# Performance work log

Hardware: AMD Instinct MI355X
Metric: run time of the kernel (lower is better)

Reference implementation:

```python
import jax, jax.numpy as jnp
import numpy as np

B, N, K = 2, 8192, 16
D_IN, D_OUT = 32, 128
EPS = 1e-5


def _bn(x, gamma, beta):
    # x: (B, C, L); BatchNorm1d training-mode stats over (B, L)
    mean = x.mean(axis=(0, 2), keepdims=True)
    var = x.var(axis=(0, 2), keepdims=True)
    return gamma[None, :, None] * (x - mean) * jax.lax.rsqrt(var + EPS) + beta[None, :, None]


def _shared_mlp(x, w, b, gamma, beta, act):
    # SharedMLP: 1x1 Conv1d (channel GEMM) + BN + activation. x: (B, Cin, L)
    y = jnp.einsum('oi,bil->bol', w, x) + b[None, :, None]
    return act(_bn(y, gamma, beta))


def _attentive_pool(x, w, b):
    # x: (B, C, N, K); per-(b,n,k) Linear over C, softmax over K, weighted sum over K
    scores = jnp.einsum('oc,bcnk->bonk', w, x) + b[None, :, None, None]
    scores = jax.nn.softmax(scores, axis=-1)
    return jnp.sum(scores * x, axis=-1)  # (B, C, N)  (torch keeps K=1 dim; squeezed by SharedMLP reshape)


def _knn(coords, k):
    # brute-force squared-L2 KNN excluding self (faiss IndexFlatL2 semantics)
    sq = jnp.sum(coords * coords, axis=-1)  # (B, N)
    d2 = sq[:, :, None] + sq[:, None, :] - 2.0 * jnp.einsum('bid,bjd->bij', coords, coords)
    n = coords.shape[1]
    d2 = jnp.where(jnp.eye(n, dtype=bool)[None], jnp.inf, d2)
    neg, idx = jax.lax.top_k(-d2, k)  # ascending squared distance
    return idx, jnp.maximum(-neg, 0.0)


def _lse(coords, features, idx, dist, w, b, gamma, beta):
    # LocalSpatialEncoding: gather neighbor coords, build 10-ch relative features, MLP, concat
    Bq, Nq, Kq = idx.shape
    neighbor = jax.vmap(lambda c, i: c[i])(coords, idx)  # (B, N, K, 3)
    center = jnp.broadcast_to(coords[:, :, None, :], neighbor.shape)
    rel = center - neighbor
    spatial = jnp.concatenate([center, neighbor, rel, dist[..., None]], axis=-1)  # (B, N, K, 10)
    spatial = spatial.transpose(0, 3, 1, 2).reshape(Bq, 10, Nq * Kq)
    sf = _shared_mlp(spatial, w, b, gamma, beta, jax.nn.relu).reshape(Bq, -1, Nq, Kq)
    feat = jnp.broadcast_to(features[..., None], (Bq, features.shape[1], Nq, Kq))
    return jnp.concatenate([sf, feat], axis=1)


def _forward(coords, features,
             mlp1_w, mlp1_b, mlp1_g, mlp1_bt,
             lse1_w, lse1_b, lse1_g, lse1_bt,
             mlpp1_w, mlpp1_b, mlpp1_g, mlpp1_bt,
             lse2_w, lse2_b, lse2_g, lse2_bt,
             mlp2_w, mlp2_b, mlp2_g, mlp2_bt,
             res_w, res_b, res_g, res_bt,
             pool1_w, pool1_b, pool2_w, pool2_b):
    # faiss output is detached in torch (numpy round-trip) -> stop_gradient
    idx, dist = _knn(jax.lax.stop_gradient(coords), K)
    lrelu02 = lambda v: jnp.where(v >= 0, v, 0.2 * v)   # LeakyReLU(0.2)
    lrelu01 = lambda v: jnp.where(v >= 0, v, 0.01 * v)  # default LeakyReLU
    x = _shared_mlp(features, mlp1_w, mlp1_b, mlp1_g, mlp1_bt, lrelu02)      # (B, 64, N)
    x = _lse(coords, x, idx, dist, lse1_w, lse1_b, lse1_g, lse1_bt)          # (B, 128, N, K)
    x = _attentive_pool(x, pool1_w, pool1_b)                                  # (B, 128, N)
    x = _shared_mlp(x, mlpp1_w, mlpp1_b, mlpp1_g, mlpp1_bt, jax.nn.relu)     # (B, 32, N)
    x = _lse(coords, x, idx, dist, lse2_w, lse2_b, lse2_g, lse2_bt)          # (B, 64, N, K)
    x = _attentive_pool(x, pool2_w, pool2_b)                                  # (B, 64, N)
    x_main = _shared_mlp(x, mlp2_w, mlp2_b, mlp2_g, mlp2_bt, jax.nn.relu)    # (B, 128, N)
    resid = _shared_mlp(features, res_w, res_b, res_g, res_bt, jax.nn.relu)  # (B, 128, N)
    return lrelu01(jnp.concatenate([x_main, resid], axis=1))                 # (B, 256, N)


def setup_inputs() -> dict:
    key = jax.random.key(0)
    ks = iter(jax.random.split(key, 64))

    def lin(ci, co):
        w = jax.random.normal(next(ks), (co, ci), jnp.float32) / np.float32(np.sqrt(ci))
        b = jax.random.normal(next(ks), (co,), jnp.float32) * 0.01
        return w, b

    inp = {}
    inp['coords'] = jax.random.normal(next(ks), (B, N, 3), jnp.float32)
    inp['features'] = jax.random.normal(next(ks), (B, D_IN, N), jnp.float32)
    for name, ci, co in [('mlp1', D_IN, D_OUT // 2), ('lse1', 10, D_OUT // 2),
                         ('mlpp1', D_OUT, D_OUT // 4), ('lse2', 10, D_OUT // 4),
                         ('mlp2', D_OUT // 2, D_OUT), ('res', D_IN, D_OUT)]:
        w, b = lin(ci, co)
        inp[name + '_w'], inp[name + '_b'] = w, b
        inp[name + '_g'] = jnp.ones((co,), jnp.float32)
        inp[name + '_bt'] = jnp.zeros((co,), jnp.float32)
    for name, c in [('pool1', D_OUT), ('pool2', D_OUT // 2)]:
        w, b = lin(c, c)
        inp[name + '_w'], inp[name + '_b'] = w, b
    return inp


def reference(coords, features,
              mlp1_w, mlp1_b, mlp1_g, mlp1_bt,
              lse1_w, lse1_b, lse1_g, lse1_bt,
              mlpp1_w, mlpp1_b, mlpp1_g, mlpp1_bt,
              lse2_w, lse2_b, lse2_g, lse2_bt,
              mlp2_w, mlp2_b, mlp2_g, mlp2_bt,
              res_w, res_b, res_g, res_bt,
              pool1_w, pool1_b, pool2_w, pool2_b):
    return _forward(coords, features,
                    mlp1_w, mlp1_b, mlp1_g, mlp1_bt,
                    lse1_w, lse1_b, lse1_g, lse1_bt,
                    mlpp1_w, mlpp1_b, mlpp1_g, mlpp1_bt,
                    lse2_w, lse2_b, lse2_g, lse2_bt,
                    mlp2_w, mlp2_b, mlp2_g, mlp2_bt,
                    res_w, res_b, res_g, res_bt,
                    pool1_w, pool1_b, pool2_w, pool2_b)
```

## Files before the change

### kernel.cpp

```cpp
#include <hip/hip_runtime.h>

static constexpr int N_ = 8192;
static constexpr int B_ = 2;
static constexpr int K_ = 16;

typedef __attribute__((ext_vector_type(8))) short bf16x8;
typedef __attribute__((ext_vector_type(4))) float f32x4;

__device__ __forceinline__ short f2bf(float f) {
  unsigned int u = __float_as_uint(f);
  unsigned int r = (u + 0x7FFFu + ((u >> 16) & 1u)) >> 16;
  return (short)r;
}
__device__ __forceinline__ float bf2f(short h) {
  return __uint_as_float(((unsigned int)(unsigned short)h) << 16);
}

__global__ __launch_bounds__(512) void knn_kernel(const float* __restrict__ coords,
                                                  int* __restrict__ oidx,
                                                  float* __restrict__ odist) {
  __shared__ float4 pts[2048];
  const int b = blockIdx.y;
  const int wv = threadIdx.x >> 6;
  const int lane = threadIdx.x & 63;
  const int q0 = blockIdx.x * 16 + wv * 2;
  const int q1 = q0 + 1;
  const float* cb = coords + (size_t)b * N_ * 3;
  const float qx0 = cb[q0 * 3 + 0], qy0 = cb[q0 * 3 + 1], qz0 = cb[q0 * 3 + 2];
  const float qx1 = cb[q1 * 3 + 0], qy1 = cb[q1 * 3 + 1], qz1 = cb[q1 * 3 + 2];
  const float qsq0 = __fadd_rn(__fadd_rn(__fmul_rn(qx0, qx0), __fmul_rn(qy0, qy0)), __fmul_rn(qz0, qz0));
  const float qsq1 = __fadd_rn(__fadd_rn(__fmul_rn(qx1, qx1), __fmul_rn(qy1, qy1)), __fmul_rn(qz1, qz1));
  const int up_addr = (lane > 0 ? lane - 1 : 0) << 2;
  float kd0 = INFINITY, kd1 = INFINITY;
  int ki0 = 0, ki1 = 0;
  float tau0 = INFINITY, tau1 = INFINITY;
  for (int t0 = 0; t0 < N_; t0 += 2048) {
    __syncthreads();
    for (int i = threadIdx.x; i < 2048; i += 512) {
      const int p = t0 + i;
      const float x = cb[p * 3 + 0], y = cb[p * 3 + 1], z = cb[p * 3 + 2];
      const float sq = __fadd_rn(__fadd_rn(__fmul_rn(x, x), __fmul_rn(y, y)), __fmul_rn(z, z));
      pts[i] = make_float4(x, y, z, sq);
    }
    __syncthreads();
    for (int s = 0; s < 2048; s += 64) {
      const float4 p = pts[s + lane];
      float d20, d21;
      {
        const float dot = __fadd_rn(__fadd_rn(__fmul_rn(qx0, p.x), __fmul_rn(qy0, p.y)), __fmul_rn(qz0, p.z));
        d20 = __fsub_rn(__fadd_rn(qsq0, p.w), __fmul_rn(2.0f, dot));
      }
      {
        const float dot = __fadd_rn(__fadd_rn(__fmul_rn(qx1, p.x), __fmul_rn(qy1, p.y)), __fmul_rn(qz1, p.z));
        d21 = __fsub_rn(__fadd_rn(qsq1, p.w), __fmul_rn(2.0f, dot));
      }
      unsigned long long m0 = __ballot(d20 < tau0);
      unsigned long long m1 = __ballot(d21 < tau1);
      const int base = t0 + s;
      if (base == (q0 & ~63)) m0 &= ~(1ull << (q0 & 63));
      if (base == (q1 & ~63)) m1 &= ~(1ull << (q1 & 63));
      while (m0 | m1) {
        if (m0) {
          const int src = __builtin_ctzll(m0);
          const float dc = __uint_as_float(__builtin_amdgcn_readlane(__float_as_uint(d20), src));
          const int jc = base + src;
          const float sd = __uint_as_float(__builtin_amdgcn_ds_bpermute(up_addr, __float_as_uint(kd0)));
          const int si = __builtin_amdgcn_ds_bpermute(up_addr, ki0);
          const bool c1 = kd0 > dc;
          const bool c2 = (lane > 0) && (sd > dc);
          kd0 = c1 ? (c2 ? sd : dc) : kd0;
          ki0 = c1 ? (c2 ? si : jc) : ki0;
          m0 &= (m0 - 1);
          tau0 = __uint_as_float(__builtin_amdgcn_readlane(__float_as_uint(kd0), 15));
          m0 &= __ballot(d20 < tau0);
        }
        if (m1) {
          const int src = __builtin_ctzll(m1);
          const float dc = __uint_as_float(__builtin_amdgcn_readlane(__float_as_uint(d21), src));
          const int jc = base + src;
          const float sd = __uint_as_float(__builtin_amdgcn_ds_bpermute(up_addr, __float_as_uint(kd1)));
          const int si = __builtin_amdgcn_ds_bpermute(up_addr, ki1);
          const bool c1 = kd1 > dc;
          const bool c2 = (lane > 0) && (sd > dc);
          kd1 = c1 ? (c2 ? sd : dc) : kd1;
          ki1 = c1 ? (c2 ? si : jc) : ki1;
          m1 &= (m1 - 1);
          tau1 = __uint_as_float(__builtin_amdgcn_readlane(__float_as_uint(kd1), 15));
          m1 &= __ballot(d21 < tau1);
        }
      }
    }
  }
  if (lane < 16) {
    oidx[((size_t)b * N_ + q0) * K_ + lane] = ki0;
    odist[((size_t)b * N_ + q0) * K_ + lane] = fmaxf(kd0, 0.0f);
    oidx[((size_t)b * N_ + q1) * K_ + lane] = ki1;
    odist[((size_t)b * N_ + q1) * K_ + lane] = fmaxf(kd1, 0.0f);
  }
}

__global__ __launch_bounds__(64) void moments_kernel(const float* __restrict__ coords,
                                                     const int* __restrict__ knn_i,
                                                     const float* __restrict__ knn_d,
                                                     double* __restrict__ mom) {
  const int t = blockIdx.x * 64 + threadIdx.x;
  const int b = t >> 13, n = t & (N_ - 1);
  float acc[65];
#pragma unroll
  for (int e = 0; e < 65; ++e) acc[e] = 0.0f;
  const float* cb = coords + (size_t)b * N_ * 3;
  const float cx = cb[n * 3 + 0], cy = cb[n * 3 + 1], cz = cb[n * 3 + 2];
  for (int k = 0; k < K_; ++k) {
    const int id = knn_i[(size_t)t * K_ + k];
    const float dd = knn_d[(size_t)t * K_ + k];
    const float nx = cb[id * 3 + 0], ny = cb[id * 3 + 1], nz = cb[id * 3 + 2];
    const float s[10] = {cx, cy, cz, nx, ny, nz, cx - nx, cy - ny, cz - nz, dd};
    int e = 0;
#pragma unroll
    for (int i = 0; i < 10; ++i) acc[e++] += s[i];
#pragma unroll
    for (int i = 0; i < 10; ++i)
#pragma unroll
      for (int jj = i; jj < 10; ++jj) acc[e++] += s[i] * s[jj];
  }
#pragma unroll
  for (int e = 0; e < 65; ++e) {
    float v = acc[e];
#pragma unroll
    for (int off = 32; off > 0; off >>= 1) v += __shfl_xor(v, off);
    acc[e] = v;
  }
  __shared__ float buf[65];
  if (threadIdx.x == 0) {
#pragma unroll
    for (int e = 0; e < 65; ++e) buf[e] = acc[e];
  }
  __syncthreads();
  if (threadIdx.x < 64) atomicAdd(&mom[threadIdx.x], (double)buf[threadIdx.x]);
  if (threadIdx.x == 0) atomicAdd(&mom[64], (double)buf[64]);
}

__device__ __forceinline__ void convert_frags(const float* __restrict__ w, short* __restrict__ H,
                                              short* __restrict__ L, int CI, int CO, int tid) {
  const int NT = CO / 16;
  for (int i = tid; i < CI * CO; i += 256) {
    const int j = i & 7, l = (i >> 3) & 63, tmp = i >> 9;
    const int tt = tmp % NT, cc = tmp / NT;
    const int c = cc * 32 + (l >> 4) * 8 + j;
    const int o = tt * 16 + (l & 15);
    const float v = w[o * CI + c];
    const short h = f2bf(v);
    H[i] = h;
    L[i] = f2bf(v - bf2f(h));
  }
}

__global__ void setup_kernel(const double* __restrict__ mom,
                             const float* __restrict__ w1, const float* __restrict__ b1,
                             const float* __restrict__ g1, const float* __restrict__ t1,
                             const float* __restrict__ w2, const float* __restrict__ b2,
                             const float* __restrict__ g2, const float* __restrict__ t2,
                             float* __restrict__ w1f, float* __restrict__ b1f,
                             float* __restrict__ w2f, float* __restrict__ b2f,
                             const float* __restrict__ pw1, const float* __restrict__ pw2,
                             short* __restrict__ wB1, short* __restrict__ wB2,
                             const float* __restrict__ wm1, short* __restrict__ f1H, short* __restrict__ f1L,
                             const float* __restrict__ wmp, short* __restrict__ f2H, short* __restrict__ f2L,
                             const float* __restrict__ wm2, short* __restrict__ f3H, short* __restrict__ f3L,
                             const float* __restrict__ wrs, short* __restrict__ fRH, short* __restrict__ fRL) {
  const int t = threadIdx.x;
  for (int i = t; i < 128 * 128; i += 256) wB1[i] = f2bf(pw1[i]);
  for (int i = t; i < 64 * 64; i += 256) wB2[i] = f2bf(pw2[i]);
  convert_frags(wm1, f1H, f1L, 32, 64, t);
  convert_frags(wmp, f2H, f2L, 128, 32, t);
  convert_frags(wm2, f3H, f3L, 64, 128, t);
  convert_frags(wrs, fRH, fRL, 32, 128, t);
  __shared__ double mu[10];
  __shared__ double S[10][10];
  const double cnt = (double)B_ * N_ * K_;
  if (t < 10) mu[t] = mom[t] / cnt;
  if (t < 55) {
    int e = t, i = 0;
    while (e >= 10 - i) { e -= 10 - i; ++i; }
    const int j = i + e;
    const double v = mom[10 + t] / cnt;
    S[i][j] = v;
    S[j][i] = v;
  }
  __syncthreads();
  const float *w, *bias, *gg, *bt;
  float *wf, *bf;
  int c;
  if (t < 64) { w = w1; bias = b1; gg = g1; bt = t1; wf = w1f; bf = b1f; c = t; }
  else if (t < 96) { w = w2; bias = b2; gg = g2; bt = t2; wf = w2f; bf = b2f; c = t - 64; }
  else return;
  double wd[10];
#pragma unroll
  for (int d = 0; d < 10; ++d) wd[d] = (double)w[c * 10 + d];
  const double cbv = (double)bias[c];
  double mz = cbv;
  for (int d = 0; d < 10; ++d) mz += wd[d] * mu[d];
  double e2 = cbv * cbv;
  for (int d = 0; d < 10; ++d) e2 += 2.0 * cbv * wd[d] * mu[d];
  for (int d = 0; d < 10; ++d)
    for (int e = 0; e < 10; ++e) e2 += wd[d] * wd[e] * S[d][e];
  const double var = e2 - mz * mz;
  const double a = (double)gg[c] / sqrt(var + 1e-5);
  const double shift = (double)bt[c] - a * mz;
#pragma unroll
  for (int d = 0; d < 10; ++d) wf[c * 10 + d] = (float)(a * wd[d]);
  bf[c] = (float)(a * cbv + shift);
}

template <int CI, int CO, bool ROWMAJ>
__global__ __launch_bounds__(256) void gemm_mfma_kernel(const float* __restrict__ in,
                                                        const short* __restrict__ fragH,
                                                        const short* __restrict__ fragL,
                                                        const float* __restrict__ bias,
                                                        float* __restrict__ out,
                                                        double* __restrict__ sacc) {
  constexpr int NT = CO / 16;
  constexpr int NC = CI / 32;
  __shared__ float part[4][CO][2];
  const int wv = threadIdx.x >> 6, l = threadIdx.x & 63;
  const int col = l & 15, quad = l >> 4;
  const int p0 = blockIdx.x * 64 + wv * 16;
  const int pt = p0 + col;
  f32x4 d[NT];
#pragma unroll
  for (int t = 0; t < NT; ++t) {
    const float bv = bias[t * 16 + col];
    d[t][0] = bv; d[t][1] = bv; d[t][2] = bv; d[t][3] = bv;
  }
#pragma unroll
  for (int cc = 0; cc < NC; ++cc) {
    float xv[8];
    if (ROWMAJ) {
      const float* ip = in + (size_t)pt * CI + cc * 32 + quad * 8;
      *(float4*)&xv[0] = *(const float4*)ip;
      *(float4*)&xv[4] = *(const float4*)(ip + 4);
    } else {
      const int b = pt >> 13, n = pt & (N_ - 1);
      const float* ip = in + ((size_t)b * CI + cc * 32 + quad * 8) * N_ + n;
#pragma unroll
      for (int j = 0; j < 8; ++j) xv[j] = ip[(size_t)j * N_];
    }
    union { bf16x8 v; short u[8]; } AH, AL;
#pragma unroll
    for (int j = 0; j < 8; ++j) {
      const short h = f2bf(xv[j]);
      AH.u[j] = h;
      AL.u[j] = f2bf(xv[j] - bf2f(h));
    }
#pragma unroll
    for (int t = 0; t < NT; ++t) {
      const size_t fo = ((size_t)(cc * NT + t) * 64 + l) * 8;
      const bf16x8 BH = *(const bf16x8*)(fragH + fo);
      const bf16x8 BL = *(const bf16x8*)(fragL + fo);
      d[t] = __builtin_amdgcn_mfma_f32_16x16x32_bf16(AH.v, BH, d[t], 0, 0, 0);
      d[t] = __builtin_amdgcn_mfma_f32_16x16x32_bf16(AH.v, BL, d[t], 0, 0, 0);
      d[t] = __builtin_amdgcn_mfma_f32_16x16x32_bf16(AL.v, BH, d[t], 0, 0, 0);
    }
  }
#pragma unroll
  for (int t = 0; t < NT; ++t) {
#pragma unroll
    for (int r = 0; r < 4; ++r)
      out[(size_t)(p0 + quad * 4 + r) * CO + t * 16 + col] = d[t][r];
    float s1 = d[t][0] + d[t][1] + d[t][2] + d[t][3];
    float s2 = d[t][0] * d[t][0] + d[t][1] * d[t][1] + d[t][2] * d[t][2] + d[t][3] * d[t][3];
    s1 += __shfl_xor(s1, 16); s1 += __shfl_xor(s1, 32);
    s2 += __shfl_xor(s2, 16); s2 += __shfl_xor(s2, 32);
    if (quad == 0) { part[wv][t * 16 + col][0] = s1; part[wv][t * 16 + col][1] = s2; }
  }
  __syncthreads();
  if (threadIdx.x < CO) {
    const int o = threadIdx.x;
    atomicAdd(&sacc[o], (double)(part[0][o][0] + part[1][o][0] + part[2][o][0] + part[3][o][0]));
    atomicAdd(&sacc[CO + o], (double)(part[0][o][1] + part[1][o][1] + part[2][o][1] + part[3][o][1]));
  }
}

template <int CSF, int CF>
__global__ __launch_bounds__(256) void pool_kernel(
    const float* __restrict__ coords, const int* __restrict__ knn_i, const float* __restrict__ knn_d,
    const float* __restrict__ wlse, const float* __restrict__ blse,
    const float* __restrict__ feat, const double* __restrict__ sfe,
    const float* __restrict__ gfe, const float* __restrict__ tfe,
    const float slope,
    const short* __restrict__ wB, const float* __restrict__ pb,
    float* __restrict__ out) {
  constexpr int C = CSF + CF;
  constexpr int CP = C + 4;
  constexpr int NT = C / 16;
  constexpr int NC = C / 32;
  __shared__ float xcat[4][16][CP];
  __shared__ float sp[4][10][16];
  const int g = threadIdx.x >> 6;
  const int l = threadIdx.x & 63;
  const int quad = l >> 4, col = l & 15;
  const int pid = blockIdx.x * 4 + g;
  const int b = pid >> 13, n = pid & (N_ - 1);
  const float* cb = coords + (size_t)b * N_ * 3;

  if (l < 16) {
    const int id = knn_i[(size_t)pid * K_ + l];
    const float dd = knn_d[(size_t)pid * K_ + l];
    const float cx = cb[n * 3 + 0], cy = cb[n * 3 + 1], cz = cb[n * 3 + 2];
    const float nx = cb[id * 3 + 0], ny = cb[id * 3 + 1], nz = cb[id * 3 + 2];
    sp[g][0][l] = cx; sp[g][1][l] = cy; sp[g][2][l] = cz;
    sp[g][3][l] = nx; sp[g][4][l] = ny; sp[g][5][l] = nz;
    sp[g][6][l] = cx - nx; sp[g][7][l] = cy - ny; sp[g][8][l] = cz - nz;
    sp[g][9][l] = dd;
  }
  if (l < CF) {
    const double cnt = (double)(B_ * N_);
    const double mean = sfe[l] / cnt;
    const double var = sfe[CF + l] / cnt - mean * mean;
    const double av = (double)gfe[l] / sqrt(var + 1e-5);
    const float af = (float)av;
    const float bfv = (float)((double)tfe[l] - av * mean);
    float v = feat[(size_t)pid * CF + l];
    v = af * v + bfv;
    v = (v >= 0.0f) ? v : slope * v;
#pragma unroll
    for (int j = 0; j < 16; ++j) xcat[g][j][CSF + l] = v;
  }
  __syncthreads();
  if (l < CSF) {
    float z[16];
    const float bz = blse[l];
#pragma unroll
    for (int j = 0; j < 16; ++j) z[j] = bz;
#pragma unroll
    for (int d = 0; d < 10; ++d) {
      const float wv = wlse[l * 10 + d];
      const float4* sr = (const float4*)&sp[g][d][0];
      const float4 s0 = sr[0], s1 = sr[1], s2 = sr[2], s3 = sr[3];
      z[0] += wv * s0.x; z[1] += wv * s0.y; z[2] += wv * s0.z; z[3] += wv * s0.w;
      z[4] += wv * s1.x; z[5] += wv * s1.y; z[6] += wv * s1.z; z[7] += wv * s1.w;
      z[8] += wv * s2.x; z[9] += wv * s2.y; z[10] += wv * s2.z; z[11] += wv * s2.w;
      z[12] += wv * s3.x; z[13] += wv * s3.y; z[14] += wv * s3.z; z[15] += wv * s3.w;
    }
#pragma unroll
    for (int j = 0; j < 16; ++j) xcat[g][j][l] = fmaxf(z[j], 0.0f);
  }
  __syncthreads();
  f32x4 d[NT];
#pragma unroll
  for (int t = 0; t < NT; ++t) {
    const float pbv = pb[t * 16 + col];
    d[t][0] = pbv; d[t][1] = pbv; d[t][2] = pbv; d[t][3] = pbv;
  }
#pragma unroll
  for (int cc = 0; cc < NC; ++cc) {
    const float* xr = &xcat[g][col][cc * 32 + quad * 8];
    const float4 xa = *(const float4*)xr;
    const float4 xb = *(const float4*)(xr + 4);
    union { bf16x8 v; short u[8]; } A;
    A.u[0] = f2bf(xa.x); A.u[1] = f2bf(xa.y); A.u[2] = f2bf(xa.z); A.u[3] = f2bf(xa.w);
    A.u[4] = f2bf(xb.x); A.u[5] = f2bf(xb.y); A.u[6] = f2bf(xb.z); A.u[7] = f2bf(xb.w);
#pragma unroll
    for (int t = 0; t < NT; ++t) {
      const bf16x8 Bv = *(const bf16x8*)(wB + (size_t)(t * 16 + col) * C + cc * 32 + quad * 8);
      d[t] = __builtin_amdgcn_mfma_f32_16x16x32_bf16(A.v, Bv, d[t], 0, 0, 0);
    }
  }
#pragma unroll
  for (int t = 0; t < NT; ++t) {
    float mx = fmaxf(fmaxf(d[t][0], d[t][1]), fmaxf(d[t][2], d[t][3]));
    mx = fmaxf(mx, __shfl_xor(mx, 16));
    mx = fmaxf(mx, __shfl_xor(mx, 32));
    float e0 = __expf(d[t][0] - mx), e1 = __expf(d[t][1] - mx);
    float e2 = __expf(d[t][2] - mx), e3 = __expf(d[t][3] - mx);
    float s = e0 + e1 + e2 + e3;
    s += __shfl_xor(s, 16);
    s += __shfl_xor(s, 32);
    const int o = t * 16 + col;
    float part = e0 * xcat[g][quad * 4 + 0][o] + e1 * xcat[g][quad * 4 + 1][o] +
                 e2 * xcat[g][quad * 4 + 2][o] + e3 * xcat[g][quad * 4 + 3][o];
    part += __shfl_xor(part, 16);
    part += __shfl_xor(part, 32);
    if (quad == 0) out[(size_t)pid * C + o] = part / s;
  }
}

__global__ __launch_bounds__(256) void final_kernel(const float* __restrict__ y3,
                                                    const float* __restrict__ yr,
                                                    const double* __restrict__ s3,
                                                    const float* __restrict__ g3, const float* __restrict__ t3,
                                                    const double* __restrict__ sr,
                                                    const float* __restrict__ gr, const float* __restrict__ tr,
                                                    float* __restrict__ out) {
  __shared__ float tile[256 * 17];
  const int blk = blockIdx.x;
  const int b = blk >> 9;
  const int n0 = (blk & 511) << 4;
  const int c = threadIdx.x;
  const float* src;
  const double* sa;
  const float *gp, *tp;
  int cc;
  if (c < 128) { src = y3; sa = s3; gp = g3; tp = t3; cc = c; }
  else { src = yr; sa = sr; gp = gr; tp = tr; cc = c - 128; }
  const double cnt = (double)(B_ * N_);
  const double mean = sa[cc] / cnt;
  const double var = sa[128 + cc] / cnt - mean * mean;
  const double avd = (double)gp[cc] / sqrt(var + 1e-5);
  const float av = (float)avd;
  const float bv = (float)((double)tp[cc] - avd * mean);
#pragma unroll
  for (int nl = 0; nl < 16; ++nl) {
    const float x = av * src[((size_t)(b * N_ + n0 + nl)) * 128 + cc] + bv;
    tile[c * 17 + nl] = fmaxf(x, 0.0f);
  }
  __syncthreads();
  const int np = c & 15, grp = c >> 4;
#pragma unroll
  for (int j = 0; j < 16; ++j) {
    const int c2 = grp * 16 + j;
    out[((size_t)(b * 256 + c2)) * N_ + n0 + np] = tile[c2 * 17 + np];
  }
}

extern "C" void kernel_launch(void* const* d_in, const int* in_sizes, int n_in,
                              void* d_out, int out_size, void* d_ws, size_t ws_size,
                              hipStream_t stream) {
  (void)in_sizes; (void)n_in; (void)out_size; (void)ws_size;
  const float* coords   = (const float*)d_in[0];
  const float* features = (const float*)d_in[1];
  const float* mlp1_w = (const float*)d_in[2];
  const float* mlp1_b = (const float*)d_in[3];
  const float* mlp1_g = (const float*)d_in[4];
  const float* mlp1_t = (const float*)d_in[5];
  const float* lse1_w = (const float*)d_in[6];
  const float* lse1_b = (const float*)d_in[7];
  const float* lse1_g = (const float*)d_in[8];
  const float* lse1_t = (const float*)d_in[9];
  const float* mlpp1_w = (const float*)d_in[10];
  const float* mlpp1_b = (const float*)d_in[11];
  const float* mlpp1_g = (const float*)d_in[12];
  const float* mlpp1_t = (const float*)d_in[13];
  const float* lse2_w = (const float*)d_in[14];
  const float* lse2_b = (const float*)d_in[15];
  const float* lse2_g = (const float*)d_in[16];
  const float* lse2_t = (const float*)d_in[17];
  const float* mlp2_w = (const float*)d_in[18];
  const float* mlp2_b = (const float*)d_in[19];
  const float* mlp2_g = (const float*)d_in[20];
  const float* mlp2_t = (const float*)d_in[21];
  const float* res_w = (const float*)d_in[22];
  const float* res_b = (const float*)d_in[23];
  const float* res_g = (const float*)d_in[24];
  const float* res_t = (const float*)d_in[25];
  const float* pool1_w = (const float*)d_in[26];
  const float* pool1_b = (const float*)d_in[27];
  const float* pool2_w = (const float*)d_in[28];
  const float* pool2_b = (const float*)d_in[29];

  float* wsf = (float*)d_ws;
  int* knn_i = (int*)d_ws;
  float* knn_d = wsf + 262144;
  float* y1 = wsf + 524288;
  float* pooled1 = wsf + 1572864;
  float* y2 = wsf + 3670016;
  float* pooled2 = wsf + 4194304;
  float* y3 = wsf + 5242880;
  float* yr = wsf + 7340032;
  double* dacc = (double*)(wsf + 9437184);
  double* mom = dacc;
  double* sacc_mlp1 = dacc + 65;
  double* sacc_mlpp1 = dacc + 193;
  double* sacc_mlp2 = dacc + 257;
  double* sacc_res = dacc + 513;
  float* fpar = wsf + 9437184 + 1600;
  float* w1f = fpar;
  float* b1f = w1f + 640;
  float* w2f = b1f + 64;
  float* b2f = w2f + 320;
  short* wB1 = (short*)(b2f + 32);
  short* wB2 = wB1 + 16384;
  short* f1H = wB2 + 4096;
  short* f1L = f1H + 2048;
  short* f2H = f1L + 2048;
  short* f2L = f2H + 4096;
  short* f3H = f2L + 4096;
  short* f3L = f3H + 8192;
  short* fRH = f3L + 8192;
  short* fRL = fRH + 4096;

  hipMemsetAsync(dacc, 0, 769 * sizeof(double), stream);
  knn_kernel<<<dim3(N_ / 16, B_), 512, 0, stream>>>(coords, knn_i, knn_d);
  moments_kernel<<<256, 64, 0, stream>>>(coords, knn_i, knn_d, mom);
  setup_kernel<<<1, 256, 0, stream>>>(mom, lse1_w, lse1_b, lse1_g, lse1_t,
                                      lse2_w, lse2_b, lse2_g, lse2_t,
                                      w1f, b1f, w2f, b2f, pool1_w, pool2_w, wB1, wB2,
                                      mlp1_w, f1H, f1L, mlpp1_w, f2H, f2L,
                                      mlp2_w, f3H, f3L, res_w, fRH, fRL);
  gemm_mfma_kernel<32, 64, false><<<256, 256, 0, stream>>>(features, f1H, f1L, mlp1_b, y1, sacc_mlp1);
  pool_kernel<64, 64><<<B_ * N_ / 4, 256, 0, stream>>>(
      coords, knn_i, knn_d, w1f, b1f, y1, sacc_mlp1, mlp1_g, mlp1_t, 0.2f, wB1, pool1_b, pooled1);
  gemm_mfma_kernel<128, 32, true><<<256, 256, 0, stream>>>(pooled1, f2H, f2L, mlpp1_b, y2, sacc_mlpp1);
  pool_kernel<32, 32><<<B_ * N_ / 4, 256, 0, stream>>>(
      coords, knn_i, knn_d, w2f, b2f, y2, sacc_mlpp1, mlpp1_g, mlpp1_t, 0.0f, wB2, pool2_b, pooled2);
  gemm_mfma_kernel<64, 128, true><<<256, 256, 0, stream>>>(pooled2, f3H, f3L, mlp2_b, y3, sacc_mlp2);
  gemm_mfma_kernel<32, 128, false><<<256, 256, 0, stream>>>(features, fRH, fRL, res_b, yr, sacc_res);
  final_kernel<<<B_ * 512, 256, 0, stream>>>(y3, yr, sacc_mlp2, mlp2_g, mlp2_t,
                                             sacc_res, res_g, res_t, (float*)d_out);
}
```

Measured before the change: 464.0 us.

## Use DPP shifts in KNN insert, factor moments, split weight conversion kernel

The KNN insertion loop replaces ds_bpermute lane shifts with DPP row shifts and splits the interleaved two-query loop into two separate loops. The moments kernel accumulates a few per-point neighbor sums and rebuilds the 65 second moments algebraically, instead of accumulating all 65 products per neighbor. Weight bf16 fragment conversion moves out of the single-block setup kernel into a 28-block convert kernel, and setup now runs with 128 threads. Risks: DPP row_shr shifts only within 16-lane rows, so lane 16 no longer receives lane 15's value. That breaks the shift semantics only for lanes at or beyond 16, which are never output. The algebraic moment expansion changes float rounding.

```diff
diff --git a/kernel.cpp b/kernel.cpp
--- a/kernel.cpp
+++ b/kernel.cpp
@@ -14,6 +14,16 @@
 }
 __device__ __forceinline__ float bf2f(short h) {
   return __uint_as_float(((unsigned int)(unsigned short)h) << 16);
+}
+__device__ __forceinline__ float dpp_shr1_f(float x) {
+  return __uint_as_float((unsigned int)__builtin_amdgcn_update_dpp(
+      0, (int)__float_as_uint(x), 0x111, 0xF, 0xF, true));
+}
+__device__ __forceinline__ int dpp_shr1_i(int x) {
+  return __builtin_amdgcn_update_dpp(0, x, 0x111, 0xF, 0xF, true);
+}
+__device__ __forceinline__ float rdlane_f(float x, int l) {
+  return __uint_as_float(__builtin_amdgcn_readlane(__float_as_uint(x), l));
 }
 
 __global__ __launch_bounds__(512) void knn_kernel(const float* __restrict__ coords,
@@ -23,6 +33,7 @@
   const int b = blockIdx.y;
   const int wv = threadIdx.x >> 6;
   const int lane = threadIdx.x & 63;
+  const bool lpos = (lane != 0);
   const int q0 = blockIdx.x * 16 + wv * 2;
   const int q1 = q0 + 1;
   const float* cb = coords + (size_t)b * N_ * 3;
@@ -30,7 +41,6 @@
   const float qx1 = cb[q1 * 3 + 0], qy1 = cb[q1 * 3 + 1], qz1 = cb[q1 * 3 + 2];
   const float qsq0 = __fadd_rn(__fadd_rn(__fmul_rn(qx0, qx0), __fmul_rn(qy0, qy0)), __fmul_rn(qz0, qz0));
   const float qsq1 = __fadd_rn(__fadd_rn(__fmul_rn(qx1, qx1), __fmul_rn(qy1, qy1)), __fmul_rn(qz1, qz1));
-  const int up_addr = (lane > 0 ? lane - 1 : 0) << 2;
   float kd0 = INFINITY, kd1 = INFINITY;
   int ki0 = 0, ki1 = 0;
   float tau0 = INFINITY, tau1 = INFINITY;
@@ -45,6 +55,7 @@
     __syncthreads();
     for (int s = 0; s < 2048; s += 64) {
       const float4 p = pts[s + lane];
+      const int base = t0 + s;
       float d20, d21;
       {
         const float dot = __fadd_rn(__fadd_rn(__fmul_rn(qx0, p.x), __fmul_rn(qy0, p.y)), __fmul_rn(qz0, p.z));
@@ -56,38 +67,35 @@
       }
       unsigned long long m0 = __ballot(d20 < tau0);
       unsigned long long m1 = __ballot(d21 < tau1);
-      const int base = t0 + s;
       if (base == (q0 & ~63)) m0 &= ~(1ull << (q0 & 63));
       if (base == (q1 & ~63)) m1 &= ~(1ull << (q1 & 63));
-      while (m0 | m1) {
-        if (m0) {
-          const int src = __builtin_ctzll(m0);
-          const float dc = __uint_as_float(__builtin_amdgcn_readlane(__float_as_uint(d20), src));
-          const int jc = base + src;
-          const float sd = __uint_as_float(__builtin_amdgcn_ds_bpermute(up_addr, __float_as_uint(kd0)));
-          const int si = __builtin_amdgcn_ds_bpermute(up_addr, ki0);
-          const bool c1 = kd0 > dc;
-          const bool c2 = (lane > 0) && (sd > dc);
-          kd0 = c1 ? (c2 ? sd : dc) : kd0;
-          ki0 = c1 ? (c2 ? si : jc) : ki0;
-          m0 &= (m0 - 1);
-          tau0 = __uint_as_float(__builtin_amdgcn_readlane(__float_as_uint(kd0), 15));
-          m0 &= __ballot(d20 < tau0);
-        }
-        if (m1) {
-          const int src = __builtin_ctzll(m1);
-          const float dc = __uint_as_float(__builtin_amdgcn_readlane(__float_as_uint(d21), src));
-          const int jc = base + src;
-          const float sd = __uint_as_float(__builtin_amdgcn_ds_bpermute(up_addr, __float_as_uint(kd1)));
-          const int si = __builtin_amdgcn_ds_bpermute(up_addr, ki1);
-          const bool c1 = kd1 > dc;
-          const bool c2 = (lane > 0) && (sd > dc);
-          kd1 = c1 ? (c2 ? sd : dc) : kd1;
-          ki1 = c1 ? (c2 ? si : jc) : ki1;
-          m1 &= (m1 - 1);
-          tau1 = __uint_as_float(__builtin_amdgcn_readlane(__float_as_uint(kd1), 15));
-          m1 &= __ballot(d21 < tau1);
-        }
+      while (m0) {
+        const int src = __builtin_ctzll(m0);
+        const float dc = rdlane_f(d20, src);
+        const int jc = base + src;
+        const float sd = dpp_shr1_f(kd0);
+        const int si = dpp_shr1_i(ki0);
+        const bool c1 = kd0 > dc;
+        const bool c2 = lpos && (sd > dc);
+        kd0 = c1 ? (c2 ? sd : dc) : kd0;
+        ki0 = c1 ? (c2 ? si : jc) : ki0;
+        m0 &= (m0 - 1);
+        tau0 = rdlane_f(kd0, 15);
+        m0 &= __ballot(d20 < tau0);
+      }
+      while (m1) {
+        const int src = __builtin_ctzll(m1);
+        const float dc = rdlane_f(d21, src);
+        const int jc = base + src;
+        const float sd = dpp_shr1_f(kd1);
+        const int si = dpp_shr1_i(ki1);
+        const bool c1 = kd1 > dc;
+        const bool c2 = lpos && (sd > dc);
+        kd1 = c1 ? (c2 ? sd : dc) : kd1;
+        ki1 = c1 ? (c2 ? si : jc) : ki1;
+        m1 &= (m1 - 1);
+        tau1 = rdlane_f(kd1, 15);
+        m1 &= __ballot(d21 < tau1);
       }
     }
   }
@@ -97,6 +105,34 @@
     oidx[((size_t)b * N_ + q1) * K_ + lane] = ki1;
     odist[((size_t)b * N_ + q1) * K_ + lane] = fmaxf(kd1, 0.0f);
   }
+}
+
+__device__ __forceinline__ float snn_get(const float* SNN, int a, int b) {
+  const int i = a < b ? a : b, j = a < b ? b : a;
+  return SNN[i == 0 ? j : (i == 1 ? 2 + j : 3 + j)];
+}
+__device__ __forceinline__ float mom_mean(int i, const float* C, const float* SN, float Sd) {
+  if (i < 3) return 16.0f * C[i];
+  if (i < 6) return SN[i - 3];
+  if (i < 9) return 16.0f * C[i - 6] - SN[i - 6];
+  return Sd;
+}
+__device__ __forceinline__ float mom_prod(int i, int j, const float* C, const float* SN,
+                                          const float* SNN, float Sd, float Sdd, const float* SND) {
+  const int ti = i < 3 ? 0 : (i < 6 ? 1 : (i < 9 ? 2 : 3));
+  const int tj = j < 3 ? 0 : (j < 6 ? 1 : (j < 9 ? 2 : 3));
+  const int a = (ti == 3) ? 0 : (i - ti * 3);
+  const int bb = (tj == 3) ? 0 : (j - tj * 3);
+  if (ti == 0 && tj == 0) return 16.0f * C[a] * C[bb];
+  if (ti == 0 && tj == 1) return C[a] * SN[bb];
+  if (ti == 0 && tj == 2) return C[a] * (16.0f * C[bb] - SN[bb]);
+  if (ti == 0 && tj == 3) return C[a] * Sd;
+  if (ti == 1 && tj == 1) return snn_get(SNN, a, bb);
+  if (ti == 1 && tj == 2) return C[bb] * SN[a] - snn_get(SNN, a, bb);
+  if (ti == 1 && tj == 3) return SND[a];
+  if (ti == 2 && tj == 2) return 16.0f * C[a] * C[bb] - C[a] * SN[bb] - C[bb] * SN[a] + snn_get(SNN, a, bb);
+  if (ti == 2 && tj == 3) return C[a] * Sd - SND[a];
+  return Sdd;
 }
 
 __global__ __launch_bounds__(64) void moments_kernel(const float* __restrict__ coords,
@@ -105,45 +141,50 @@
                                                      double* __restrict__ mom) {
   const int t = blockIdx.x * 64 + threadIdx.x;
   const int b = t >> 13, n = t & (N_ - 1);
-  float acc[65];
-#pragma unroll
-  for (int e = 0; e < 65; ++e) acc[e] = 0.0f;
   const float* cb = coords + (size_t)b * N_ * 3;
-  const float cx = cb[n * 3 + 0], cy = cb[n * 3 + 1], cz = cb[n * 3 + 2];
+  float C[3] = {cb[n * 3 + 0], cb[n * 3 + 1], cb[n * 3 + 2]};
+  float SN[3] = {0.f, 0.f, 0.f}, SNN[6] = {0.f, 0.f, 0.f, 0.f, 0.f, 0.f};
+  float SND[3] = {0.f, 0.f, 0.f}, Sd = 0.f, Sdd = 0.f;
   for (int k = 0; k < K_; ++k) {
     const int id = knn_i[(size_t)t * K_ + k];
     const float dd = knn_d[(size_t)t * K_ + k];
     const float nx = cb[id * 3 + 0], ny = cb[id * 3 + 1], nz = cb[id * 3 + 2];
-    const float s[10] = {cx, cy, cz, nx, ny, nz, cx - nx, cy - ny, cz - nz, dd};
-    int e = 0;
-#pragma unroll
-    for (int i = 0; i < 10; ++i) acc[e++] += s[i];
-#pragma unroll
-    for (int i = 0; i < 10; ++i)
-#pragma unroll
-      for (int jj = i; jj < 10; ++jj) acc[e++] += s[i] * s[jj];
-  }
-#pragma unroll
-  for (int e = 0; e < 65; ++e) {
-    float v = acc[e];
+    SN[0] += nx; SN[1] += ny; SN[2] += nz;
+    SNN[0] += nx * nx; SNN[1] += nx * ny; SNN[2] += nx * nz;
+    SNN[3] += ny * ny; SNN[4] += ny * nz; SNN[5] += nz * nz;
+    Sd += dd; Sdd += dd * dd;
+    SND[0] += nx * dd; SND[1] += ny * dd; SND[2] += nz * dd;
+  }
+  float m65[65];
+  int e = 0;
+#pragma unroll
+  for (int i = 0; i < 10; ++i) m65[e++] = mom_mean(i, C, SN, Sd);
+#pragma unroll
+  for (int i = 0; i < 10; ++i)
+#pragma unroll
+    for (int j = i; j < 10; ++j) m65[e++] = mom_prod(i, j, C, SN, SNN, Sd, Sdd, SND);
+#pragma unroll
+  for (int q = 0; q < 65; ++q) {
+    float v = m65[q];
 #pragma unroll
     for (int off = 32; off > 0; off >>= 1) v += __shfl_xor(v, off);
-    acc[e] = v;
+    m65[q] = v;
   }
   __shared__ float buf[65];
   if (threadIdx.x == 0) {
 #pragma unroll
-    for (int e = 0; e < 65; ++e) buf[e] = acc[e];
+    for (int q = 0; q < 65; ++q) buf[q] = m65[q];
   }
   __syncthreads();
   if (threadIdx.x < 64) atomicAdd(&mom[threadIdx.x], (double)buf[threadIdx.x]);
   if (threadIdx.x == 0) atomicAdd(&mom[64], (double)buf[64]);
 }
 
-__device__ __forceinline__ void convert_frags(const float* __restrict__ w, short* __restrict__ H,
-                                              short* __restrict__ L, int CI, int CO, int tid) {
-  const int NT = CO / 16;
-  for (int i = tid; i < CI * CO; i += 256) {
+template <int CI, int CO>
+__device__ __forceinline__ void conv_frag_seg(const float* __restrict__ w, short* __restrict__ H,
+                                              short* __restrict__ L, int tid, int nthr) {
+  constexpr int NT = CO / 16;
+  for (int i = tid; i < CI * CO; i += nthr) {
     const int j = i & 7, l = (i >> 3) & 63, tmp = i >> 9;
     const int tt = tmp % NT, cc = tmp / NT;
     const int c = cc * 32 + (l >> 4) * 8 + j;
@@ -155,26 +196,39 @@
   }
 }
 
+__global__ __launch_bounds__(256) void convert_kernel(
+    const float* __restrict__ pw1, const float* __restrict__ pw2,
+    short* __restrict__ wB1, short* __restrict__ wB2,
+    const float* __restrict__ wm1, short* __restrict__ f1H, short* __restrict__ f1L,
+    const float* __restrict__ wmp, short* __restrict__ f2H, short* __restrict__ f2L,
+    const float* __restrict__ wm2, short* __restrict__ f3H, short* __restrict__ f3L,
+    const float* __restrict__ wrs, short* __restrict__ fRH, short* __restrict__ fRL) {
+  const int blk = blockIdx.x;
+  if (blk < 8) {
+    const int tid = blk * 256 + threadIdx.x;
+    for (int i = tid; i < 128 * 128; i += 2048) wB1[i] = f2bf(pw1[i]);
+  } else if (blk < 10) {
+    const int tid = (blk - 8) * 256 + threadIdx.x;
+    for (int i = tid; i < 64 * 64; i += 512) wB2[i] = f2bf(pw2[i]);
+  } else if (blk < 12) {
+    conv_frag_seg<32, 64>(wm1, f1H, f1L, (blk - 10) * 256 + threadIdx.x, 512);
+  } else if (blk < 16) {
+    conv_frag_seg<128, 32>(wmp, f2H, f2L, (blk - 12) * 256 + threadIdx.x, 1024);
+  } else if (blk < 24) {
+    conv_frag_seg<64, 128>(wm2, f3H, f3L, (blk - 16) * 256 + threadIdx.x, 2048);
+  } else {
+    conv_frag_seg<32, 128>(wrs, fRH, fRL, (blk - 24) * 256 + threadIdx.x, 1024);
+  }
+}
+
 __global__ void setup_kernel(const double* __restrict__ mom,
                              const float* __restrict__ w1, const float* __restrict__ b1,
                              const float* __restrict__ g1, const float* __restrict__ t1,
                              const float* __restrict__ w2, const float* __restrict__ b2,
                              const float* __restrict__ g2, const float* __restrict__ t2,
                              float* __restrict__ w1f, float* __restrict__ b1f,
-                             float* __restrict__ w2f, float* __restrict__ b2f,
-                             const float* __restrict__ pw1, const float* __restrict__ pw2,
-                             short* __restrict__ wB1, short* __restrict__ wB2,
-                             const float* __restrict__ wm1, short* __restrict__ f1H, short* __restrict__ f1L,
-                             const float* __restrict__ wmp, short* __restrict__ f2H, short* __restrict__ f2L,
-                             const float* __restrict__ wm2, short* __restrict__ f3H, short* __restrict__ f3L,
-                             const float* __restrict__ wrs, short* __restrict__ fRH, short* __restrict__ fRL) {
+                             float* __restrict__ w2f, float* __restrict__ b2f) {
   const int t = threadIdx.x;
-  for (int i = t; i < 128 * 128; i += 256) wB1[i] = f2bf(pw1[i]);
-  for (int i = t; i < 64 * 64; i += 256) wB2[i] = f2bf(pw2[i]);
-  convert_frags(wm1, f1H, f1L, 32, 64, t);
-  convert_frags(wmp, f2H, f2L, 128, 32, t);
-  convert_frags(wm2, f3H, f3L, 64, 128, t);
-  convert_frags(wrs, fRH, fRL, 32, 128, t);
   __shared__ double mu[10];
   __shared__ double S[10][10];
   const double cnt = (double)B_ * N_ * K_;
@@ -491,12 +545,13 @@
 
   hipMemsetAsync(dacc, 0, 769 * sizeof(double), stream);
   knn_kernel<<<dim3(N_ / 16, B_), 512, 0, stream>>>(coords, knn_i, knn_d);
+  convert_kernel<<<28, 256, 0, stream>>>(pool1_w, pool2_w, wB1, wB2,
+                                         mlp1_w, f1H, f1L, mlpp1_w, f2H, f2L,
+                                         mlp2_w, f3H, f3L, res_w, fRH, fRL);
   moments_kernel<<<256, 64, 0, stream>>>(coords, knn_i, knn_d, mom);
-  setup_kernel<<<1, 256, 0, stream>>>(mom, lse1_w, lse1_b, lse1_g, lse1_t,
+  setup_kernel<<<1, 128, 0, stream>>>(mom, lse1_w, lse1_b, lse1_g, lse1_t,
                                       lse2_w, lse2_b, lse2_g, lse2_t,
-                                      w1f, b1f, w2f, b2f, pool1_w, pool2_w, wB1, wB2,
-                                      mlp1_w, f1H, f1L, mlpp1_w, f2H, f2L,
-                                      mlp2_w, f3H, f3L, res_w, fRH, fRL);
+                                      w1f, b1f, w2f, b2f);
   gemm_mfma_kernel<32, 64, false><<<256, 256, 0, stream>>>(features, f1H, f1L, mlp1_b, y1, sacc_mlp1);
   pool_kernel<64, 64><<<B_ * N_ / 4, 256, 0, stream>>>(
       coords, knn_i, knn_d, w1f, b1f, y1, sacc_mlp1, mlp1_g, mlp1_t, 0.2f, wB1, pool1_b, pooled1);
```

Result: faster. 434.9 us (-6.3%).
